# Kernel tuning notes

Hardware: AMD Instinct MI355X
Metric: run time of the kernel (lower is better)

Reference implementation:

```python
import jax, jax.numpy as jnp
import numpy as np

N_BASIS = 16
CUTOFF = 5.0
S3 = 3.0 ** 0.5


def _cg_121():
    # Real Clebsch-Gordan for 1o x 2e -> 1o built from the equivariant map
    # (v, T) -> T @ v where T is the traceless symmetric matrix encoded by the
    # 5 real l=2 components (e3nn y-principal convention). Normalized to unit
    # Frobenius norm (wigner-3j-like normalization).
    s15 = np.sqrt(15.0); s5 = np.sqrt(5.0)
    C = np.zeros((3, 3, 5))
    for j in range(5):
        c = np.zeros(5); c[j] = 1.0
        T = np.zeros((3, 3))
        T[0, 2] = T[2, 0] = c[0] / s15
        T[0, 1] = T[1, 0] = c[1] / s15
        T[1, 2] = T[2, 1] = c[3] / s15
        Tyy = 2.0 * c[2] / (3.0 * s5)
        T[1, 1] = Tyy
        T[2, 2] = -Tyy / 2.0 + c[4] / s15
        T[0, 0] = -Tyy / 2.0 - c[4] / s15
        C[:, :, j] = T
    C /= np.linalg.norm(C)
    return jnp.asarray(C, dtype=jnp.float32)


def _sph(n):
    # component-normalized real spherical harmonics l=0,1,2 of unit vectors n [E,3]
    x, y, z = n[:, 0], n[:, 1], n[:, 2]
    Y0 = jnp.ones_like(x)
    Y1 = S3 * n  # [E,3]
    s15 = 15.0 ** 0.5; s5 = 5.0 ** 0.5
    Y2 = jnp.stack([s15 * x * z, s15 * x * y, 0.5 * s5 * (3 * y * y - 1.0),
                    s15 * y * z, 0.5 * s15 * (z * z - x * x)], axis=-1)  # [E,5]
    return Y0, Y1, Y2


def _tfn_forward(x, pos, W1, W2, edge_index, cg121):
    row, col = edge_index[0], edge_index[1]
    E = row.shape[0]
    N = pos.shape[0]
    ev = pos[row] - pos[col]                         # [E,3]
    d = jnp.sqrt(jnp.sum(ev * ev, axis=-1) + 1e-12)  # [E]
    n = ev / d[:, None]
    # Gaussian radial basis, 16 centers on [0, cutoff]
    mu = jnp.linspace(0.0, CUTOFF, N_BASIS)
    delta = CUTOFF / (N_BASIS - 1)
    rbf = jnp.exp(-((d[:, None] - mu) ** 2) / (2.0 * delta * delta))  # [E,16]
    # normalized 2-layer MLP -> per-edge TP weights [E, 576]
    h = jax.nn.relu((rbf @ W1) / jnp.sqrt(16.0))
    w = (h @ W2) / jnp.sqrt(64.0)
    Y0, Y1, Y2 = _sph(n)
    ss = jnp.stack([Y0, Y0], axis=-1)   # [E,2]  2x0e
    sv = jnp.stack([Y1, Y1], axis=1)    # [E,2,3] 2x1o
    st = Y2                              # [E,5]  1x2e
    xs = x[row, :8]                      # [E,8]  8x0e
    xv = x[row, 8:].reshape(E, 8, 3)     # [E,8,3] 8x1o
    wA = w[:, 0:128].reshape(E, 8, 2, 8)
    wB = w[:, 128:256].reshape(E, 8, 2, 8)
    wC = w[:, 256:384].reshape(E, 8, 2, 8)
    wD = w[:, 384:512].reshape(E, 8, 2, 8)
    wE = w[:, 512:576].reshape(E, 8, 8)
    a0 = 1.0 / jnp.sqrt(32.0)            # sqrt(2*0+1)/sqrt(fan_in=32)
    a1 = jnp.sqrt(3.0) / jnp.sqrt(40.0)  # sqrt(2*1+1)/sqrt(fan_in=40)
    out_s = a0 * (jnp.einsum('euvw,eu,ev->ew', wA, xs, ss)
                  + jnp.einsum('euvw,eui,evi->ew', wB, xv, sv) / S3)
    out_v = a1 * (jnp.einsum('euvw,eu,evk->ewk', wC, xs, sv) / S3
                  + jnp.einsum('euvw,euk,ev->ewk', wD, xv, ss) / S3
                  + jnp.einsum('euw,eui,ej,kij->ewk', wE, xv, st, cg121))
    out = jnp.concatenate([out_s, out_v.reshape(E, 24)], axis=-1)  # [E,32]
    y = jax.ops.segment_sum(out, row, num_segments=N)              # [N,32]
    # gate: silu on scalar (l=0) channels only
    return jnp.concatenate([jax.nn.silu(y[:, :8]), y[:, 8:]], axis=-1)


def setup_inputs() -> dict:
    key = jax.random.key(0)
    k1, k2, k3, k4, k5 = jax.random.split(key, 5)
    N, E = 25000, 400000
    x = jax.random.normal(k1, (N, 32), dtype=jnp.float32)
    pos = jax.random.normal(k2, (N, 3), dtype=jnp.float32)
    edge_index = jax.random.randint(k3, (2, E), 0, N, dtype=jnp.int64 if jax.config.read('jax_enable_x64') else jnp.int32)
    W1 = jax.random.normal(k4, (16, 64), dtype=jnp.float32)
    W2 = jax.random.normal(k5, (64, 576), dtype=jnp.float32)
    return {"x": x, "pos": pos, "edge_index": edge_index, "W1": W1, "W2": W2}


def reference(x, pos, edge_index, W1, W2):
    cg121 = _cg_121()
    return _tfn_forward(x, pos, W1, W2, edge_index, cg121)
```

## Files before the change

### kernel.cpp

```cpp
#include <hip/hip_runtime.h>
#include <hip/hip_fp16.h>


#define INV_S3  0.5773502691896258f
#define A0S     0.1767766952966369f
#define A1S     0.27386127875258306f
#define S15     3.872983346207417f
#define S5      2.23606797749979f
#define INV_S10 0.31622776601683794f
#define INV_S30 0.18257418583505536f

#define TBL   2048
#define DMAX  8.0f
#define CAP   128

typedef _Float16 half8 __attribute__((ext_vector_type(8)));

__global__ __launch_bounds__(256) void prep_all(
    const float* __restrict__ W1, const float* __restrict__ W2,
    const int* __restrict__ ei, _Float16* __restrict__ T,
    int* __restrict__ cnt, int* __restrict__ scol, int E) {

    __shared__ float hs[4][64];
    int tid = threadIdx.x;
    int wv = tid >> 6, lane = tid & 63;
    int j = blockIdx.x * 4 + wv;

    float hv = 0.f;
    if (j < TBL) {
        float d = (float)j * (DMAX / (float)(TBL - 1));
        float acc = 0.f;
#pragma unroll
        for (int i = 0; i < 16; ++i) {
            float t = d - (float)i * (1.0f / 3.0f);
            float r = __expf(-4.5f * t * t);
            acc = fmaf(r, W1[i * 64 + lane], acc);
        }
        hv = fmaxf(acc, 0.f) * 0.25f;
    }
    hs[wv][lane] = hv;
    __syncthreads();

    if (j < TBL) {
        int u = lane >> 3, wo = lane & 7;
        int b0 = u * 16 + wo;
        int b4 = 512 + u * 8 + wo;
        float a0 = 0.f, a1 = 0.f, a2 = 0.f, a3 = 0.f, a4 = 0.f;
#pragma unroll 4
        for (int k = 0; k < 64; ++k) {
            float hk = hs[wv][k];
            const float* Wk = W2 + k * 576;
            a0 = fmaf(hk, Wk[b0]       + Wk[b0 + 8],       a0);
            a1 = fmaf(hk, Wk[128 + b0] + Wk[128 + b0 + 8], a1);
            a2 = fmaf(hk, Wk[256 + b0] + Wk[256 + b0 + 8], a2);
            a3 = fmaf(hk, Wk[384 + b0] + Wk[384 + b0 + 8], a3);
            a4 = fmaf(hk, Wk[b4], a4);
        }
        _Float16* Tr = T + (size_t)j * 320;
        Tr[lane]        = (_Float16)a0;
        Tr[64 + lane]   = (_Float16)a1;
        Tr[128 + lane]  = (_Float16)a2;
        Tr[192 + lane]  = (_Float16)a3;
        Tr[256 + lane]  = (_Float16)a4;
    }

    int gtid = blockIdx.x * 256 + tid;
    int gsz = gridDim.x * 256;
    for (int e = gtid; e < E; e += gsz) {
        int row = ei[e];
        int p = atomicAdd(&cnt[row], 1);
        if (p < CAP) scol[(size_t)row * CAP + p] = ei[E + e];
    }
}

__global__ __launch_bounds__(256) void tfn_node(
    const float* __restrict__ x, const float* __restrict__ pos,
    const int* __restrict__ scol, const int* __restrict__ cnt,
    const _Float16* __restrict__ T, float* __restrict__ y, int N) {

    int wv = threadIdx.x >> 6, lane = threadIdx.x & 63;
    int n = blockIdx.x * 4 + wv;
    if (n >= N) return;

    int g = lane >> 3;
    int u = lane & 7;
    int kc = cnt[n];
    if (kc > CAP) kc = CAP;
    const int* nbr = scol + (size_t)n * CAP;

    const float* xr = x + (size_t)n * 32;
    float xu  = xr[u];
    float xv0 = xr[8 + 3 * u + 0];
    float xv1 = xr[8 + 3 * u + 1];
    float xv2 = xr[8 + 3 * u + 2];
    float prx = pos[3 * n + 0], pry = pos[3 * n + 1], prz = pos[3 * n + 2];

    float V[32];
#pragma unroll
    for (int z = 0; z < 32; ++z) V[z] = 0.f;

    int rounds = (kc + 7) >> 3;
    for (int rd = 0; rd < rounds; ++rd) {
        int slot = rd * 8 + g;
        if (slot < kc) {
            int col = nbr[slot];
            float evx = prx - pos[3 * col + 0];
            float evy = pry - pos[3 * col + 1];
            float evz = prz - pos[3 * col + 2];
            float d2 = evx * evx + evy * evy + evz * evz + 1e-12f;
            float invd = rsqrtf(d2);
            float dd = d2 * invd;
            float nx = evx * invd, ny = evy * invd, nz = evz * invd;

            float fj = dd * ((float)(TBL - 1) / DMAX);
            int j0 = (int)fj;
            j0 = min(j0, TBL - 2);
            float tf = fminf(fj - (float)j0, 1.0f);
            _Float16 th = (_Float16)tf;

            const _Float16* Ar = T + (size_t)j0 * 320 + u * 8;
            half8 A[5], B[5];
#pragma unroll
            for (int t = 0; t < 5; ++t) {
                A[t] = *(const half8*)(Ar + t * 64);
                B[t] = *(const half8*)(Ar + 320 + t * 64);
            }

            float qu = xv0 * nx + xv1 * ny + xv2 * nz;
            float Y22 = 0.5f * S5 * (3.f * ny * ny - 1.f);
            float Y24 = 0.5f * S15 * (nz * nz - nx * nx);
            float M00 = -Y22 * INV_S30 - Y24 * INV_S10;
            float M11 = 2.f * Y22 * INV_S30;
            float M22 = -Y22 * INV_S30 + Y24 * INV_S10;
            float M01 = (S15 * nx * ny) * INV_S10;
            float M02 = (S15 * nx * nz) * INV_S10;
            float M12 = (S15 * ny * nz) * INV_S10;
            float m0 = M00 * xv0 + M01 * xv1 + M02 * xv2;
            float m1 = M01 * xv0 + M11 * xv1 + M12 * xv2;
            float m2 = M02 * xv0 + M12 * xv1 + M22 * xv2;

#pragma unroll
            for (int t = 0; t < 5; ++t) {
                half8 w;
#pragma unroll
                for (int z = 0; z < 8; ++z)
                    w[z] = A[t][z] + (B[t][z] - A[t][z]) * th;
                if (t == 0) {
#pragma unroll
                    for (int z = 0; z < 8; ++z) V[z] = fmaf(xu, (float)w[z], V[z]);
                } else if (t == 1) {
#pragma unroll
                    for (int z = 0; z < 8; ++z) V[z] = fmaf(qu, (float)w[z], V[z]);
                } else if (t == 2) {
#pragma unroll
                    for (int z = 0; z < 8; ++z) {
                        float cw = xu * (float)w[z];
                        V[8 + 3 * z]  = fmaf(cw, nx, V[8 + 3 * z]);
                        V[9 + 3 * z]  = fmaf(cw, ny, V[9 + 3 * z]);
                        V[10 + 3 * z] = fmaf(cw, nz, V[10 + 3 * z]);
                    }
                } else if (t == 3) {
#pragma unroll
                    for (int z = 0; z < 8; ++z) {
                        float wd = (float)w[z] * INV_S3;
                        V[8 + 3 * z]  = fmaf(xv0, wd, V[8 + 3 * z]);
                        V[9 + 3 * z]  = fmaf(xv1, wd, V[9 + 3 * z]);
                        V[10 + 3 * z] = fmaf(xv2, wd, V[10 + 3 * z]);
                    }
                } else {
#pragma unroll
                    for (int z = 0; z < 8; ++z) {
                        float we = (float)w[z];
                        V[8 + 3 * z]  = fmaf(m0, we, V[8 + 3 * z]);
                        V[9 + 3 * z]  = fmaf(m1, we, V[9 + 3 * z]);
                        V[10 + 3 * z] = fmaf(m2, we, V[10 + 3 * z]);
                    }
                }
            }
        }
    }

#pragma unroll
    for (int h = 16; h >= 1; h >>= 1) {
        bool hi = (lane & h) != 0;
#pragma unroll
        for (int k = 0; k < h; ++k) {
            float lo = V[k], up = V[k + h];
            float keep = hi ? up : lo;
            float send = hi ? lo : up;
            V[k] = keep + __shfl_xor(send, h, 64);
        }
    }
    V[0] += __shfl_xor(V[0], 32, 64);

    if (lane < 32) {
        float v = V[0] * 0.125f * (lane < 8 ? A0S : A1S);
        if (lane < 8) v = v / (1.0f + __expf(-v));
        y[(size_t)n * 32 + lane] = v;
    }
}

extern "C" void kernel_launch(void* const* d_in, const int* in_sizes, int n_in,
                              void* d_out, int out_size, void* d_ws, size_t ws_size,
                              hipStream_t stream) {
    const float* x   = (const float*)d_in[0];
    const float* pos = (const float*)d_in[1];
    const int*   ei  = (const int*)d_in[2];
    const float* W1  = (const float*)d_in[3];
    const float* W2  = (const float*)d_in[4];
    int N = in_sizes[1] / 3;
    int E = in_sizes[2] / 2;

    char* ws = (char*)d_ws;
    size_t off = 0;
    _Float16* T    = (_Float16*)(ws + off); off += (size_t)TBL * 320 * 2;
    int*      cnt  = (int*)(ws + off);      off += (size_t)N * 4;
    int*      scol = (int*)(ws + off);      off += (size_t)N * CAP * 4;

    float* y = (float*)d_out;

    hipMemsetAsync(cnt, 0, (size_t)N * 4, stream);
    hipLaunchKernelGGL(prep_all, dim3(TBL / 4), dim3(256), 0, stream,
                       W1, W2, ei, T, cnt, scol, E);
    hipLaunchKernelGGL(tfn_node, dim3((N + 3) / 4), dim3(256), 0, stream,
                       x, pos, scol, cnt, T, y, N);
}
```

Baseline: 151.1 us.

## Stage W2 in LDS for table build, persistent ticketed node waves with prefetch

```diff
diff --git a/kernel.cpp b/kernel.cpp
--- a/kernel.cpp
+++ b/kernel.cpp
@@ -16,56 +16,51 @@
 
 typedef _Float16 half8 __attribute__((ext_vector_type(8)));
 
-__global__ __launch_bounds__(256) void prep_all(
+__global__ __launch_bounds__(320) void prep_all(
     const float* __restrict__ W1, const float* __restrict__ W2,
     const int* __restrict__ ei, _Float16* __restrict__ T,
     int* __restrict__ cnt, int* __restrict__ scol, int E) {
 
-    __shared__ float hs[4][64];
+    __shared__ float w2s[64 * 320];
+    __shared__ float hs[64];
     int tid = threadIdx.x;
-    int wv = tid >> 6, lane = tid & 63;
-    int j = blockIdx.x * 4 + wv;
-
-    float hv = 0.f;
-    if (j < TBL) {
+    int bid = blockIdx.x;
+
+    {
+        int t = tid >> 6, r = tid & 63;
+        int u = r >> 3, wo = r & 7;
+        int src = (t < 4) ? (t * 128 + u * 16 + wo) : (512 + u * 8 + wo);
+        bool twin = (t < 4);
+        for (int k = 0; k < 64; ++k) {
+            float v = W2[k * 576 + src];
+            if (twin) v += W2[k * 576 + src + 8];
+            w2s[k * 320 + tid] = v;
+        }
+    }
+
+    for (int jj = 0; jj < 8; ++jj) {
+        int j = bid * 8 + jj;
         float d = (float)j * (DMAX / (float)(TBL - 1));
+        __syncthreads();
+        if (tid < 64) {
+            float acc = 0.f;
+#pragma unroll
+            for (int i = 0; i < 16; ++i) {
+                float t = d - (float)i * (1.0f / 3.0f);
+                float r = __expf(-4.5f * t * t);
+                acc = fmaf(r, W1[i * 64 + tid], acc);
+            }
+            hs[tid] = fmaxf(acc, 0.f) * 0.25f;
+        }
+        __syncthreads();
         float acc = 0.f;
-#pragma unroll
-        for (int i = 0; i < 16; ++i) {
-            float t = d - (float)i * (1.0f / 3.0f);
-            float r = __expf(-4.5f * t * t);
-            acc = fmaf(r, W1[i * 64 + lane], acc);
-        }
-        hv = fmaxf(acc, 0.f) * 0.25f;
-    }
-    hs[wv][lane] = hv;
-    __syncthreads();
-
-    if (j < TBL) {
-        int u = lane >> 3, wo = lane & 7;
-        int b0 = u * 16 + wo;
-        int b4 = 512 + u * 8 + wo;
-        float a0 = 0.f, a1 = 0.f, a2 = 0.f, a3 = 0.f, a4 = 0.f;
-#pragma unroll 4
-        for (int k = 0; k < 64; ++k) {
-            float hk = hs[wv][k];
-            const float* Wk = W2 + k * 576;
-            a0 = fmaf(hk, Wk[b0]       + Wk[b0 + 8],       a0);
-            a1 = fmaf(hk, Wk[128 + b0] + Wk[128 + b0 + 8], a1);
-            a2 = fmaf(hk, Wk[256 + b0] + Wk[256 + b0 + 8], a2);
-            a3 = fmaf(hk, Wk[384 + b0] + Wk[384 + b0 + 8], a3);
-            a4 = fmaf(hk, Wk[b4], a4);
-        }
-        _Float16* Tr = T + (size_t)j * 320;
-        Tr[lane]        = (_Float16)a0;
-        Tr[64 + lane]   = (_Float16)a1;
-        Tr[128 + lane]  = (_Float16)a2;
-        Tr[192 + lane]  = (_Float16)a3;
-        Tr[256 + lane]  = (_Float16)a4;
-    }
-
-    int gtid = blockIdx.x * 256 + tid;
-    int gsz = gridDim.x * 256;
+#pragma unroll 8
+        for (int k = 0; k < 64; ++k) acc = fmaf(hs[k], w2s[k * 320 + tid], acc);
+        T[(size_t)j * 320 + tid] = (_Float16)acc;
+    }
+
+    int gtid = bid * 320 + tid;
+    int gsz = gridDim.x * 320;
     for (int e = gtid; e < E; e += gsz) {
         int row = ei[e];
         int p = atomicAdd(&cnt[row], 1);
@@ -76,127 +71,150 @@
 __global__ __launch_bounds__(256) void tfn_node(
     const float* __restrict__ x, const float* __restrict__ pos,
     const int* __restrict__ scol, const int* __restrict__ cnt,
-    const _Float16* __restrict__ T, float* __restrict__ y, int N) {
-
-    int wv = threadIdx.x >> 6, lane = threadIdx.x & 63;
-    int n = blockIdx.x * 4 + wv;
-    if (n >= N) return;
-
+    const _Float16* __restrict__ T, int* __restrict__ ticket,
+    float* __restrict__ y, int N) {
+
+    int lane = threadIdx.x & 63;
     int g = lane >> 3;
     int u = lane & 7;
-    int kc = cnt[n];
-    if (kc > CAP) kc = CAP;
-    const int* nbr = scol + (size_t)n * CAP;
-
-    const float* xr = x + (size_t)n * 32;
-    float xu  = xr[u];
-    float xv0 = xr[8 + 3 * u + 0];
-    float xv1 = xr[8 + 3 * u + 1];
-    float xv2 = xr[8 + 3 * u + 2];
-    float prx = pos[3 * n + 0], pry = pos[3 * n + 1], prz = pos[3 * n + 2];
-
-    float V[32];
-#pragma unroll
-    for (int z = 0; z < 32; ++z) V[z] = 0.f;
-
-    int rounds = (kc + 7) >> 3;
-    for (int rd = 0; rd < rounds; ++rd) {
-        int slot = rd * 8 + g;
-        if (slot < kc) {
+
+    while (true) {
+        int tk;
+        if (lane == 0) tk = atomicAdd(ticket, 1);
+        tk = __shfl(tk, 0, 64);
+        if (tk >= N) break;
+        int n = tk;
+
+        int kc = cnt[n];
+        if (kc > CAP) kc = CAP;
+        const int* nbr = scol + (size_t)n * CAP;
+
+        const float* xr = x + (size_t)n * 32;
+        float xu  = xr[u];
+        float xv0 = xr[8 + 3 * u + 0];
+        float xv1 = xr[8 + 3 * u + 1];
+        float xv2 = xr[8 + 3 * u + 2];
+        float prx = pos[3 * n + 0], pry = pos[3 * n + 1], prz = pos[3 * n + 2];
+
+        float V[32];
+#pragma unroll
+        for (int z = 0; z < 32; ++z) V[z] = 0.f;
+
+        int rounds = (kc + 7) >> 3;
+
+        int slot = g;
+        bool val = slot < kc;
+        float evx = 0.f, evy = 0.f, evz = 0.f;
+        if (val) {
             int col = nbr[slot];
-            float evx = prx - pos[3 * col + 0];
-            float evy = pry - pos[3 * col + 1];
-            float evz = prz - pos[3 * col + 2];
-            float d2 = evx * evx + evy * evy + evz * evz + 1e-12f;
-            float invd = rsqrtf(d2);
-            float dd = d2 * invd;
-            float nx = evx * invd, ny = evy * invd, nz = evz * invd;
-
-            float fj = dd * ((float)(TBL - 1) / DMAX);
-            int j0 = (int)fj;
-            j0 = min(j0, TBL - 2);
-            float tf = fminf(fj - (float)j0, 1.0f);
-            _Float16 th = (_Float16)tf;
-
-            const _Float16* Ar = T + (size_t)j0 * 320 + u * 8;
-            half8 A[5], B[5];
-#pragma unroll
-            for (int t = 0; t < 5; ++t) {
-                A[t] = *(const half8*)(Ar + t * 64);
-                B[t] = *(const half8*)(Ar + 320 + t * 64);
-            }
-
-            float qu = xv0 * nx + xv1 * ny + xv2 * nz;
-            float Y22 = 0.5f * S5 * (3.f * ny * ny - 1.f);
-            float Y24 = 0.5f * S15 * (nz * nz - nx * nx);
-            float M00 = -Y22 * INV_S30 - Y24 * INV_S10;
-            float M11 = 2.f * Y22 * INV_S30;
-            float M22 = -Y22 * INV_S30 + Y24 * INV_S10;
-            float M01 = (S15 * nx * ny) * INV_S10;
-            float M02 = (S15 * nx * nz) * INV_S10;
-            float M12 = (S15 * ny * nz) * INV_S10;
-            float m0 = M00 * xv0 + M01 * xv1 + M02 * xv2;
-            float m1 = M01 * xv0 + M11 * xv1 + M12 * xv2;
-            float m2 = M02 * xv0 + M12 * xv1 + M22 * xv2;
-
-#pragma unroll
-            for (int t = 0; t < 5; ++t) {
-                half8 w;
-#pragma unroll
-                for (int z = 0; z < 8; ++z)
-                    w[z] = A[t][z] + (B[t][z] - A[t][z]) * th;
-                if (t == 0) {
-#pragma unroll
-                    for (int z = 0; z < 8; ++z) V[z] = fmaf(xu, (float)w[z], V[z]);
-                } else if (t == 1) {
-#pragma unroll
-                    for (int z = 0; z < 8; ++z) V[z] = fmaf(qu, (float)w[z], V[z]);
-                } else if (t == 2) {
-#pragma unroll
-                    for (int z = 0; z < 8; ++z) {
-                        float cw = xu * (float)w[z];
-                        V[8 + 3 * z]  = fmaf(cw, nx, V[8 + 3 * z]);
-                        V[9 + 3 * z]  = fmaf(cw, ny, V[9 + 3 * z]);
-                        V[10 + 3 * z] = fmaf(cw, nz, V[10 + 3 * z]);
-                    }
-                } else if (t == 3) {
-#pragma unroll
-                    for (int z = 0; z < 8; ++z) {
-                        float wd = (float)w[z] * INV_S3;
-                        V[8 + 3 * z]  = fmaf(xv0, wd, V[8 + 3 * z]);
-                        V[9 + 3 * z]  = fmaf(xv1, wd, V[9 + 3 * z]);
-                        V[10 + 3 * z] = fmaf(xv2, wd, V[10 + 3 * z]);
-                    }
-                } else {
-#pragma unroll
-                    for (int z = 0; z < 8; ++z) {
-                        float we = (float)w[z];
-                        V[8 + 3 * z]  = fmaf(m0, we, V[8 + 3 * z]);
-                        V[9 + 3 * z]  = fmaf(m1, we, V[9 + 3 * z]);
-                        V[10 + 3 * z] = fmaf(m2, we, V[10 + 3 * z]);
+            evx = prx - pos[3 * col + 0];
+            evy = pry - pos[3 * col + 1];
+            evz = prz - pos[3 * col + 2];
+        }
+
+        for (int rd = 0; rd < rounds; ++rd) {
+            bool cval = val;
+            float cex = evx, cey = evy, cez = evz;
+            slot += 8;
+            val = slot < kc;
+            if (val) {
+                int ncol = nbr[slot];
+                evx = prx - pos[3 * ncol + 0];
+                evy = pry - pos[3 * ncol + 1];
+                evz = prz - pos[3 * ncol + 2];
+            }
+            if (cval) {
+                float d2 = cex * cex + cey * cey + cez * cez + 1e-12f;
+                float invd = rsqrtf(d2);
+                float dd = d2 * invd;
+                float nx = cex * invd, ny = cey * invd, nz = cez * invd;
+
+                float fj = dd * ((float)(TBL - 1) / DMAX);
+                int j0 = (int)fj;
+                j0 = min(j0, TBL - 2);
+                float tf = fminf(fj - (float)j0, 1.0f);
+                _Float16 th = (_Float16)tf;
+
+                const _Float16* Ar = T + (size_t)j0 * 320 + u * 8;
+                half8 A[5], B[5];
+#pragma unroll
+                for (int t = 0; t < 5; ++t) {
+                    A[t] = *(const half8*)(Ar + t * 64);
+                    B[t] = *(const half8*)(Ar + 320 + t * 64);
+                }
+
+                float qu = xv0 * nx + xv1 * ny + xv2 * nz;
+                float Y22 = 0.5f * S5 * (3.f * ny * ny - 1.f);
+                float Y24 = 0.5f * S15 * (nz * nz - nx * nx);
+                float M00 = -Y22 * INV_S30 - Y24 * INV_S10;
+                float M11 = 2.f * Y22 * INV_S30;
+                float M22 = -Y22 * INV_S30 + Y24 * INV_S10;
+                float M01 = (S15 * nx * ny) * INV_S10;
+                float M02 = (S15 * nx * nz) * INV_S10;
+                float M12 = (S15 * ny * nz) * INV_S10;
+                float m0 = M00 * xv0 + M01 * xv1 + M02 * xv2;
+                float m1 = M01 * xv0 + M11 * xv1 + M12 * xv2;
+                float m2 = M02 * xv0 + M12 * xv1 + M22 * xv2;
+
+#pragma unroll
+                for (int t = 0; t < 5; ++t) {
+                    half8 w;
+#pragma unroll
+                    for (int z = 0; z < 8; ++z)
+                        w[z] = A[t][z] + (B[t][z] - A[t][z]) * th;
+                    if (t == 0) {
+#pragma unroll
+                        for (int z = 0; z < 8; ++z) V[z] = fmaf(xu, (float)w[z], V[z]);
+                    } else if (t == 1) {
+#pragma unroll
+                        for (int z = 0; z < 8; ++z) V[z] = fmaf(qu, (float)w[z], V[z]);
+                    } else if (t == 2) {
+#pragma unroll
+                        for (int z = 0; z < 8; ++z) {
+                            float cw = xu * (float)w[z];
+                            V[8 + 3 * z]  = fmaf(cw, nx, V[8 + 3 * z]);
+                            V[9 + 3 * z]  = fmaf(cw, ny, V[9 + 3 * z]);
+                            V[10 + 3 * z] = fmaf(cw, nz, V[10 + 3 * z]);
+                        }
+                    } else if (t == 3) {
+#pragma unroll
+                        for (int z = 0; z < 8; ++z) {
+                            float wd = (float)w[z] * INV_S3;
+                            V[8 + 3 * z]  = fmaf(xv0, wd, V[8 + 3 * z]);
+                            V[9 + 3 * z]  = fmaf(xv1, wd, V[9 + 3 * z]);
+                            V[10 + 3 * z] = fmaf(xv2, wd, V[10 + 3 * z]);
+                        }
+                    } else {
+#pragma unroll
+                        for (int z = 0; z < 8; ++z) {
+                            float we = (float)w[z];
+                            V[8 + 3 * z]  = fmaf(m0, we, V[8 + 3 * z]);
+                            V[9 + 3 * z]  = fmaf(m1, we, V[9 + 3 * z]);
+                            V[10 + 3 * z] = fmaf(m2, we, V[10 + 3 * z]);
+                        }
                     }
                 }
             }
         }
-    }
-
-#pragma unroll
-    for (int h = 16; h >= 1; h >>= 1) {
-        bool hi = (lane & h) != 0;
-#pragma unroll
-        for (int k = 0; k < h; ++k) {
-            float lo = V[k], up = V[k + h];
-            float keep = hi ? up : lo;
-            float send = hi ? lo : up;
-            V[k] = keep + __shfl_xor(send, h, 64);
-        }
-    }
-    V[0] += __shfl_xor(V[0], 32, 64);
-
-    if (lane < 32) {
-        float v = V[0] * 0.125f * (lane < 8 ? A0S : A1S);
-        if (lane < 8) v = v / (1.0f + __expf(-v));
-        y[(size_t)n * 32 + lane] = v;
+
+#pragma unroll
+        for (int h = 16; h >= 1; h >>= 1) {
+            bool hi = (lane & h) != 0;
+#pragma unroll
+            for (int k = 0; k < h; ++k) {
+                float lo = V[k], up = V[k + h];
+                float keep = hi ? up : lo;
+                float send = hi ? lo : up;
+                V[k] = keep + __shfl_xor(send, h, 64);
+            }
+        }
+        V[0] += __shfl_xor(V[0], 32, 64);
+
+        if (lane < 32) {
+            float v = V[0] * 0.125f * (lane < 8 ? A0S : A1S);
+            if (lane < 8) v = v / (1.0f + __expf(-v));
+            y[(size_t)n * 32 + lane] = v;
+        }
     }
 }
 
@@ -215,13 +233,14 @@
     size_t off = 0;
     _Float16* T    = (_Float16*)(ws + off); off += (size_t)TBL * 320 * 2;
     int*      cnt  = (int*)(ws + off);      off += (size_t)N * 4;
+    int*      ticket = (int*)(ws + off);    off += 64;
     int*      scol = (int*)(ws + off);      off += (size_t)N * CAP * 4;
 
     float* y = (float*)d_out;
 
-    hipMemsetAsync(cnt, 0, (size_t)N * 4, stream);
-    hipLaunchKernelGGL(prep_all, dim3(TBL / 4), dim3(256), 0, stream,
+    hipMemsetAsync(cnt, 0, (size_t)N * 4 + 64, stream);
+    hipLaunchKernelGGL(prep_all, dim3(TBL / 8), dim3(320), 0, stream,
                        W1, W2, ei, T, cnt, scol, E);
-    hipLaunchKernelGGL(tfn_node, dim3((N + 3) / 4), dim3(256), 0, stream,
-                       x, pos, scol, cnt, T, y, N);
+    hipLaunchKernelGGL(tfn_node, dim3(2048), dim3(256), 0, stream,
+                       x, pos, scol, cnt, T, ticket, y, N);
 }
```

Result: slower. 496.5 us (+228.6%).
